# Performance work log

Measured on AMD Instinct MI355X. Metric: run time of the kernel, lower is better.

The kernel has to match this reference:

```python
import jax, jax.numpy as jnp
import numpy as np

B, S, DIN, DIM, H = 2, 2304, 1024, 1024, 16
HEAD_DIM = DIM // H            # 64
ROT_DIM = HEAD_DIM             # partial_rotary_factor = 1
BASE = 10000.0
EPS = 1e-6


def setup_inputs() -> dict:
    key = jax.random.key(0)
    ks = jax.random.split(key, 6)
    return {
        "input": jax.random.normal(ks[0], (B, S, DIN), dtype=jnp.float32),
        "qkv_w": jax.random.normal(ks[1], (3 * DIM, DIN), dtype=jnp.float32) * 0.02,
        "qkv_b": jnp.zeros((3 * DIM,), dtype=jnp.float32),
        "q_scale": jnp.ones((DIM,), dtype=jnp.float32),
        "k_scale": jnp.ones((DIM,), dtype=jnp.float32),
        "proj_w": jax.random.normal(ks[2], (DIN, DIM), dtype=jnp.float32) * 0.02,
        "proj_b": jnp.zeros((DIN,), dtype=jnp.float32),
        "height": 48,
        "width": 48,
    }


def _rms_norm(x, scale):
    # RMSNorm over the full inner dim (QKNorm), learned scale
    var = jnp.mean(x * x, axis=-1, keepdims=True)
    return x * jax.lax.rsqrt(var + EPS) * scale


def _rope_1d(x, pos):
    # x: (b, n, h, d_ax), pos: (n,) float; rotate_half-style RoPE
    d = x.shape[-1]
    inv_freq = 1.0 / (BASE ** (jnp.arange(0, d, 2, dtype=jnp.float32) / d))  # (d/2,)
    ang = pos[:, None] * inv_freq                                            # (n, d/2)
    cos = jnp.concatenate([jnp.cos(ang), jnp.cos(ang)], axis=-1)[None, :, None, :]
    sin = jnp.concatenate([jnp.sin(ang), jnp.sin(ang)], axis=-1)[None, :, None, :]
    x1, x2 = jnp.split(x, 2, axis=-1)
    rot = jnp.concatenate([-x2, x1], axis=-1)
    return x * cos + rot * sin


def _rope_2d(x, height, width):
    # axial 2D RoPE: first half of rotary dims keyed by row, second half by col
    n = height * width
    idx = jnp.arange(n, dtype=jnp.float32)
    rows = jnp.floor(idx / width)
    cols = jnp.mod(idx, width)
    half = ROT_DIM // 2
    x_r = _rope_1d(x[..., :half], rows)
    x_c = _rope_1d(x[..., half:ROT_DIM], cols)
    return jnp.concatenate([x_r, x_c, x[..., ROT_DIM:]], axis=-1)


def reference(input, qkv_w, qkv_b, q_scale, k_scale, proj_w, proj_b, height, width):
    b, n, _ = input.shape
    qkv = input @ qkv_w.T + qkv_b                       # (b, n, 3*dim)
    q, k, v = jnp.split(qkv, 3, axis=-1)
    q = _rms_norm(q, q_scale)
    k = _rms_norm(k, k_scale)
    # (b, n, h, d)
    q = q.reshape(b, n, H, HEAD_DIM)
    k = k.reshape(b, n, H, HEAD_DIM)
    v = v.reshape(b, n, H, HEAD_DIM)
    q = _rope_2d(q, height, width)
    k = _rope_2d(k, height, width)
    scale = HEAD_DIM ** (-0.5)
    # (b, h, q, k)
    scores = jnp.einsum("bqhd,bkhd->bhqk", q, k) * scale
    attn = jax.nn.softmax(scores, axis=-1)
    out = jnp.einsum("bhqk,bkhd->bqhd", attn, v)        # (b, n, h, d)
    out = out.reshape(b, n, DIM)
    return out @ proj_w.T + proj_b
```

## Files before the change

kernel.cpp:

```cpp
#include <hip/hip_runtime.h>
#include <math.h>

#define BB   2
#define SS   2304
#define DINC 1024
#define DIMC 1024
#define HH   16
#define HD   64

typedef _Float16 half_t;
typedef __attribute__((ext_vector_type(4))) _Float16 half4;
typedef __attribute__((ext_vector_type(8))) _Float16 half8;
typedef __attribute__((ext_vector_type(4))) float    f32x4;

#define LOG2E 1.44269504088896340736f
#define EXP2(x) __builtin_amdgcn_exp2f(x)

#define GLOAD_LDS16(gp, lp)                                                     \
    __builtin_amdgcn_global_load_lds(                                           \
        (const __attribute__((address_space(1))) void*)(gp),                    \
        (__attribute__((address_space(3))) void*)(lp), 16, 0, 0)

template<int RB>
__global__ __launch_bounds__(256)
void convert_tile_f16(const float* __restrict__ src, half_t* __restrict__ dst, int K)
{
    constexpr int EPT = RB * 32 / 256;
    const int mb = blockIdx.x;
    const int kb = blockIdx.y;
    const int t  = threadIdx.x;
    const int e0 = t * EPT;
    const int mm = e0 >> 5;
    const int kk = e0 & 31;
    const float* sp = src + (size_t)(mb * RB + mm) * K + kb * 32 + kk;
    half_t*      dp = dst + ((size_t)mb * (K >> 5) + kb) * (RB * 32) + mm * 32 + kk;
    #pragma unroll
    for (int g = 0; g < EPT / 4; ++g) {
        float4 v = *(const float4*)(sp + 4 * g);
        dp[4 * g + 0] = (half_t)v.x; dp[4 * g + 1] = (half_t)v.y;
        dp[4 * g + 2] = (half_t)v.z; dp[4 * g + 3] = (half_t)v.w;
    }
}

template<int BN, bool OUT_HALF>
__global__ __launch_bounds__(256)
void gemm_mfma(const half_t* __restrict__ Ah, const half_t* __restrict__ Bh,
               const float* __restrict__ bias, void* __restrict__ Cout,
               int M, int N, int K)
{
    constexpr int MT = (BN == 128) ? 4 : 2;
    constexpr int NT = 4;
    const int KB = K >> 5;
    __shared__ half_t As[8192];
    __shared__ half_t Bs[2 * BN * 32];

    const int t    = threadIdx.x;
    const int w    = t >> 6;
    const int lane = t & 63;
    const int l15  = lane & 15, quad = lane >> 4;
    const int wr   = (BN == 128) ? (w >> 1) : w;
    const int wc   = (BN == 128) ? (w & 1) : 0;
    const int mb   = blockIdx.y, nb = blockIdx.x;

    f32x4 acc[MT][NT];
    #pragma unroll
    for (int mt = 0; mt < MT; ++mt)
        #pragma unroll
        for (int nt = 0; nt < NT; ++nt) acc[mt][nt] = (f32x4){0.f, 0.f, 0.f, 0.f};

    const half_t* atile = Ah + (size_t)mb * KB * 4096;
    const half_t* btile = Bh + (size_t)nb * KB * (BN * 32);

    for (int kb = 0; kb < KB; kb += 2) {
        #pragma unroll
        for (int u = 0; u < 2; ++u) {
            const half_t* at = atile + (size_t)(kb + u) * 4096;
            const half_t* bt = btile + (size_t)(kb + u) * (BN * 32);
            #pragma unroll
            for (int v = 0; v < 2; ++v) {
                const int ch = w * 2 + v;
                GLOAD_LDS16(at + ch * 512 + lane * 8, As + u * 4096 + ch * 512);
            }
            if (BN == 128) {
                #pragma unroll
                for (int v = 0; v < 2; ++v) {
                    const int ch = w * 2 + v;
                    GLOAD_LDS16(bt + ch * 512 + lane * 8, Bs + u * 4096 + ch * 512);
                }
            } else {
                GLOAD_LDS16(bt + w * 512 + lane * 8, Bs + u * (BN * 32) + w * 512);
            }
        }
        __syncthreads();

        #pragma unroll
        for (int u = 0; u < 2; ++u) {
            half8 af[MT], bf[NT];
            #pragma unroll
            for (int mt = 0; mt < MT; ++mt)
                af[mt] = *(const half8*)(As + u * 4096
                                         + (wr * (MT * 16) + mt * 16 + l15) * 32 + quad * 8);
            #pragma unroll
            for (int nt = 0; nt < NT; ++nt)
                bf[nt] = *(const half8*)(Bs + u * (BN * 32)
                                         + (wc * 64 + nt * 16 + l15) * 32 + quad * 8);
            #pragma unroll
            for (int mt = 0; mt < MT; ++mt)
                #pragma unroll
                for (int nt = 0; nt < NT; ++nt)
                    acc[mt][nt] = __builtin_amdgcn_mfma_f32_16x16x32_f16(
                        af[mt], bf[nt], acc[mt][nt], 0, 0, 0);
        }
        __syncthreads();
    }

    const int bm = mb * 128, bn = nb * BN;
    #pragma unroll
    for (int nt = 0; nt < NT; ++nt) {
        const int n  = bn + wc * 64 + nt * 16 + l15;
        const float bv = bias[n];
        #pragma unroll
        for (int mt = 0; mt < MT; ++mt) {
            const int m0 = bm + wr * (MT * 16) + mt * 16 + quad * 4;
            #pragma unroll
            for (int rg = 0; rg < 4; ++rg) {
                const float v = acc[mt][nt][rg] + bv;
                if (OUT_HALF) ((half_t*)Cout)[(size_t)(m0 + rg) * N + n] = (half_t)v;
                else          ((float*) Cout)[(size_t)(m0 + rg) * N + n] = v;
            }
        }
    }
}

__global__ __launch_bounds__(256)
void normrope_v7(half_t* __restrict__ qkvh, const float* __restrict__ q_scale,
                 const float* __restrict__ k_scale, const int* __restrict__ wptr,
                 half_t* __restrict__ Kf, half_t* __restrict__ Vf)
{
    const int token = blockIdx.x;
    const int s     = token % SS;
    const int b     = token / SS;
    const int w     = *wptr;
    const int t     = threadIdx.x;
    const float rowp = (float)(s / w);
    const float colp = (float)(s % w);

    half_t* base = qkvh + (size_t)token * 3072;

    const int c    = s >> 5;
    const int slot = s & 31;
    const int ktile = (slot >> 2) & 1;
    const int krow  = ((slot >> 3) << 2) + (slot & 3);

    {
        half4 v4 = *(const half4*)(base + 2048 + 4 * t);
        const int dabs0 = 4 * t;
        const int h  = dabs0 >> 6;
        const int sl3 = slot >> 3, sl7 = slot & 7;
        half_t* vdst = Vf + ((size_t)(b * HH + h) * 72 + c) * 2048;
        #pragma unroll
        for (int ii = 0; ii < 4; ++ii) {
            const int d = (dabs0 + ii) & 63;
            vdst[(d >> 4) * 512 + (sl3 * 16 + (d & 15)) * 8 + sl7] = v4[ii];
        }
    }

    __shared__ float buf[DIMC];
    __shared__ float red[4];

    #pragma unroll
    for (int sel = 0; sel < 2; ++sel) {
        half_t* row = base + sel * DIMC;
        const float* scp = sel ? k_scale : q_scale;

        half4 xh = *(const half4*)(row + 4 * t);
        float x0 = (float)xh[0], x1 = (float)xh[1], x2 = (float)xh[2], x3 = (float)xh[3];
        float ss = x0 * x0 + x1 * x1 + x2 * x2 + x3 * x3;
        #pragma unroll
        for (int o = 32; o >= 1; o >>= 1) ss += __shfl_xor(ss, o);
        if ((t & 63) == 0) red[t >> 6] = ss;
        __syncthreads();

        const float rinv = rsqrtf((red[0] + red[1] + red[2] + red[3]) * (1.0f / DIMC) + 1e-6f);
        float4 g = *(const float4*)(scp + 4 * t);
        buf[4 * t + 0] = x0 * rinv * g.x;
        buf[4 * t + 1] = x1 * rinv * g.y;
        buf[4 * t + 2] = x2 * rinv * g.z;
        buf[4 * t + 3] = x3 * rinv * g.w;
        __syncthreads();

        const float qsc = sel ? 1.0f : (0.125f * LOG2E);

        #pragma unroll
        for (int pp = 0; pp < 2; ++pp) {
            const int p = t + pp * 256;
            const int h = p >> 5;
            const int r = p & 31;
            const int j = r & 15;
            const float pos = (r < 16) ? rowp : colp;
            const int d1 = (r < 16) ? j : (32 + j);
            const int d2 = d1 + 16;
            const float freq = exp2f((float)j * -0.83048202372f);
            const float ang  = pos * freq;
            float sn, cs;
            __sincosf(ang, &sn, &cs);
            const float a1 = buf[h * HD + d1], a2 = buf[h * HD + d2];
            const float o1 = (a1 * cs - a2 * sn) * qsc;
            const float o2 = (a2 * cs + a1 * sn) * qsc;
            if (sel == 0) {
                row[h * HD + d1] = (half_t)o1;
                row[h * HD + d2] = (half_t)o2;
            } else {
                half_t* kdst = Kf + ((size_t)(b * HH + h) * 72 + c) * 2048;
                kdst[((ktile << 1) + (d1 >> 5)) * 512
                     + ((((d1 & 31) >> 3) << 4) + krow) * 8 + (d1 & 7)] = (half_t)o1;
                kdst[((ktile << 1) + (d2 >> 5)) * 512
                     + ((((d2 & 31) >> 3) << 4) + krow) * 8 + (d2 & 7)] = (half_t)o2;
            }
        }
        __syncthreads();
    }
}

__global__ __launch_bounds__(256, 4)
void flash_attn_mfma12(const half_t* __restrict__ qkvh, const half_t* __restrict__ Kf,
                       const half_t* __restrict__ Vf, half_t* __restrict__ attn_h)
{
    const int flat = blockIdx.x;
    const int xcd  = flat & 7;
    const int idx  = flat >> 3;
    const int bh   = xcd * 4 + idx / 36;
    const int qtb  = idx % 36;
    const int b    = bh >> 4, h = bh & 15;
    const int t    = threadIdx.x;
    const int w    = t >> 6;
    const int qh   = w >> 1;
    const int jt   = w & 1;
    const int lane = t & 63;
    const int l15  = lane & 15, quad = lane >> 4;

    const size_t tb = (size_t)b * SS;
    const int q0 = qtb * 64;

    __shared__ float mlb[4][32];
    __shared__ float Ob[2][64][33];

    half8 qf[2][2];
    #pragma unroll
    for (int qt = 0; qt < 2; ++qt)
        #pragma unroll
        for (int dg = 0; dg < 2; ++dg)
            qf[qt][dg] = *(const half8*)(qkvh + (tb + q0 + qh * 32 + qt * 16 + l15) * 3072
                                          + h * HD + dg * 32 + quad * 8);

    f32x4 acc[4][2];
    f32x4 lacc[2];
    #pragma unroll
    for (int qt = 0; qt < 2; ++qt) {
        lacc[qt] = (f32x4){0.f, 0.f, 0.f, 0.f};
        #pragma unroll
        for (int dt = 0; dt < 4; ++dt) acc[dt][qt] = (f32x4){0.f, 0.f, 0.f, 0.f};
    }

    const half_t* kpl = Kf + (size_t)bh * 147456 + jt * 2048 + lane * 8;
    const half_t* vpl = Vf + (size_t)bh * 147456 + jt * 2048 + lane * 8;

    half8 k00 = *(const half8*)(kpl);
    half8 k01 = *(const half8*)(kpl + 512);
    half8 k10 = *(const half8*)(kpl + 1024);
    half8 k11 = *(const half8*)(kpl + 1536);
    half8 v0  = *(const half8*)(vpl);
    half8 v1  = *(const half8*)(vpl + 512);
    half8 v2  = *(const half8*)(vpl + 1024);
    half8 v3  = *(const half8*)(vpl + 1536);

    const f32x4 initC = (f32x4){-4.f, -4.f, -4.f, -4.f};

    for (int p = 0; p < 36; ++p) {
        f32x4 scA[2], scB[2];
        __builtin_amdgcn_s_setprio(1);
        #pragma unroll
        for (int qt = 0; qt < 2; ++qt) {
            scA[qt] = initC;
            scA[qt] = __builtin_amdgcn_mfma_f32_16x16x32_f16(k00, qf[qt][0], scA[qt], 0, 0, 0);
            scA[qt] = __builtin_amdgcn_mfma_f32_16x16x32_f16(k01, qf[qt][1], scA[qt], 0, 0, 0);
            scB[qt] = initC;
            scB[qt] = __builtin_amdgcn_mfma_f32_16x16x32_f16(k10, qf[qt][0], scB[qt], 0, 0, 0);
            scB[qt] = __builtin_amdgcn_mfma_f32_16x16x32_f16(k11, qf[qt][1], scB[qt], 0, 0, 0);
        }
        __builtin_amdgcn_s_setprio(0);

        if (p + 1 < 36) {
            const half_t* kN = kpl + (size_t)(p + 1) * 4096;
            k00 = *(const half8*)(kN);
            k01 = *(const half8*)(kN + 512);
            k10 = *(const half8*)(kN + 1024);
            k11 = *(const half8*)(kN + 1536);
        }

        half8 pf[2];
        #pragma unroll
        for (int qt = 0; qt < 2; ++qt) {
            f32x4 eA, eB;
            #pragma unroll
            for (int rg = 0; rg < 4; ++rg) {
                eA[rg] = EXP2(scA[qt][rg]);
                eB[rg] = EXP2(scB[qt][rg]);
            }
            lacc[qt] += eA + eB;
            pf[qt] = (half8){(half_t)eA[0], (half_t)eA[1], (half_t)eA[2], (half_t)eA[3],
                             (half_t)eB[0], (half_t)eB[1], (half_t)eB[2], (half_t)eB[3]};
        }

        __builtin_amdgcn_s_setprio(1);
        #pragma unroll
        for (int dt = 0; dt < 4; ++dt) {
            const half8 vf = (dt == 0) ? v0 : (dt == 1) ? v1 : (dt == 2) ? v2 : v3;
            #pragma unroll
            for (int qt = 0; qt < 2; ++qt)
                acc[dt][qt] = __builtin_amdgcn_mfma_f32_16x16x32_f16(
                    vf, pf[qt], acc[dt][qt], 0, 0, 0);
        }
        __builtin_amdgcn_s_setprio(0);

        if (p + 1 < 36) {
            const half_t* vN = vpl + (size_t)(p + 1) * 4096;
            v0 = *(const half8*)(vN);
            v1 = *(const half8*)(vN + 512);
            v2 = *(const half8*)(vN + 1024);
            v3 = *(const half8*)(vN + 1536);
        }
    }

    #pragma unroll
    for (int qt = 0; qt < 2; ++qt) {
        float lq = (lacc[qt][0] + lacc[qt][1]) + (lacc[qt][2] + lacc[qt][3]);
        lq += __shfl_xor(lq, 16);
        lq += __shfl_xor(lq, 32);
        if (quad == 0) mlb[w][qt * 16 + l15] = lq;
    }
    __syncthreads();

    float fac[2];
    #pragma unroll
    for (int qt = 0; qt < 2; ++qt) {
        const int q = qt * 16 + l15;
        fac[qt] = 1.0f / (mlb[qh * 2 + 0][q] + mlb[qh * 2 + 1][q]);
    }

    #pragma unroll
    for (int ph = 0; ph < 2; ++ph) {
        if (jt == ph) {
            #pragma unroll
            for (int dt = 0; dt < 4; ++dt)
                #pragma unroll
                for (int qt = 0; qt < 2; ++qt)
                    #pragma unroll
                    for (int rg = 0; rg < 4; ++rg) {
                        const int d = dt * 16 + quad * 4 + rg;
                        const int q = qt * 16 + l15;
                        const float v = acc[dt][qt][rg] * fac[qt];
                        if (ph == 0) Ob[qh][d][q] = v;
                        else         Ob[qh][d][q] += v;
                    }
        }
        __syncthreads();
    }

    {
        const int q   = t >> 2;
        const int ds  = (t & 3) * 16;
        const int qh2 = q >> 5, qq = q & 31;
        const size_t mrow = tb + q0 + q;
        const int mb2 = (int)(mrow >> 7);
        const int mm  = (int)(mrow & 127);
        #pragma unroll
        for (int g = 0; g < 4; ++g) {
            const int dd = ds + 4 * g;
            const int kb2 = (h * HD + dd) >> 5;
            const int kk  = dd & 31;
            half4 o;
            o[0] = (half_t)Ob[qh2][dd + 0][qq];
            o[1] = (half_t)Ob[qh2][dd + 1][qq];
            o[2] = (half_t)Ob[qh2][dd + 2][qq];
            o[3] = (half_t)Ob[qh2][dd + 3][qq];
            *(half4*)(attn_h + ((size_t)mb2 * 32 + kb2) * 4096 + mm * 32 + kk) = o;
        }
    }
}

extern "C" void kernel_launch(void* const* d_in, const int* in_sizes, int n_in,
                              void* d_out, int out_size, void* d_ws, size_t ws_size,
                              hipStream_t stream)
{
    const float* input   = (const float*)d_in[0];
    const float* qkv_w   = (const float*)d_in[1];
    const float* qkv_b   = (const float*)d_in[2];
    const float* q_scale = (const float*)d_in[3];
    const float* k_scale = (const float*)d_in[4];
    const float* proj_w  = (const float*)d_in[5];
    const float* proj_b  = (const float*)d_in[6];
    const int*   width   = (const int*)d_in[8];
    float* out = (float*)d_out;

    half_t* qkvh   = (half_t*)d_ws;
    half_t* attn_h = qkvh   + (size_t)4608 * 3072;
    half_t* Vf     = attn_h + (size_t)4608 * 1024;
    half_t* Ah     = Vf     + (size_t)32 * 72 * 2048;
    half_t* Bh1    = Ah     + (size_t)4608 * 1024;
    half_t* Bh2    = Bh1    + (size_t)3072 * 1024;
    half_t* Kf     = Ah;

    const int M = BB * SS;

    convert_tile_f16<128><<<dim3(M / 128, DINC / 32),        256, 0, stream>>>(input,  Ah,  DINC);
    convert_tile_f16<128><<<dim3(3 * DIMC / 128, DINC / 32), 256, 0, stream>>>(qkv_w, Bh1, DINC);
    convert_tile_f16<64><<<dim3(DINC / 64, DIMC / 32),       256, 0, stream>>>(proj_w, Bh2, DIMC);

    gemm_mfma<128, true><<<dim3(3 * DIMC / 128, M / 128), 256, 0, stream>>>(
        Ah, Bh1, qkv_b, qkvh, M, 3 * DIMC, DINC);

    normrope_v7<<<M, 256, 0, stream>>>(qkvh, q_scale, k_scale, width, Kf, Vf);

    flash_attn_mfma12<<<dim3(1152), 256, 0, stream>>>(qkvh, Kf, Vf, attn_h);

    gemm_mfma<64, false><<<dim3(DINC / 64, M / 128), 256, 0, stream>>>(
        attn_h, Bh2, proj_b, out, M, DINC, DIMC);
}
```

Measured before the change: 245.3 us.

## Software-pipeline QK MFMAs ahead of PV and compute row sums via MFMA

Restructures the attention loop so that the next tile's score MFMAs are issued while the current tile's exponentials are consumed, with K fragments prefetched two iterations ahead. The softmax denominator is now accumulated with an extra MFMA against a ones-row operand instead of VALU adds and cross-lane shuffles. This aims to overlap the exp/VALU work with matrix-core work and reduce VALU load, at the cost of more live registers and two extra MFMAs per iteration.

```diff
diff --git a/kernel.cpp b/kernel.cpp
--- a/kernel.cpp
+++ b/kernel.cpp
@@ -223,7 +223,7 @@
 }
 
 __global__ __launch_bounds__(256, 4)
-void flash_attn_mfma12(const half_t* __restrict__ qkvh, const half_t* __restrict__ Kf,
+void flash_attn_mfma13(const half_t* __restrict__ qkvh, const half_t* __restrict__ Kf,
                        const half_t* __restrict__ Vf, half_t* __restrict__ attn_h)
 {
     const int flat = blockIdx.x;
@@ -253,11 +253,17 @@
             qf[qt][dg] = *(const half8*)(qkvh + (tb + q0 + qh * 32 + qt * 16 + l15) * 3072
                                           + h * HD + dg * 32 + quad * 8);
 
+    const half8 onesA = (l15 == 0)
+        ? (half8){(half_t)1, (half_t)1, (half_t)1, (half_t)1,
+                  (half_t)1, (half_t)1, (half_t)1, (half_t)1}
+        : (half8){(half_t)0, (half_t)0, (half_t)0, (half_t)0,
+                  (half_t)0, (half_t)0, (half_t)0, (half_t)0};
+
     f32x4 acc[4][2];
-    f32x4 lacc[2];
+    f32x4 acc5[2];
     #pragma unroll
     for (int qt = 0; qt < 2; ++qt) {
-        lacc[qt] = (f32x4){0.f, 0.f, 0.f, 0.f};
+        acc5[qt] = (f32x4){0.f, 0.f, 0.f, 0.f};
         #pragma unroll
         for (int dt = 0; dt < 4; ++dt) acc[dt][qt] = (f32x4){0.f, 0.f, 0.f, 0.f};
     }
@@ -276,42 +282,62 @@
 
     const f32x4 initC = (f32x4){-4.f, -4.f, -4.f, -4.f};
 
+    f32x4 scA[2], scB[2];
+    __builtin_amdgcn_s_setprio(1);
+    #pragma unroll
+    for (int qt = 0; qt < 2; ++qt) {
+        scA[qt] = initC;
+        scA[qt] = __builtin_amdgcn_mfma_f32_16x16x32_f16(k00, qf[qt][0], scA[qt], 0, 0, 0);
+        scA[qt] = __builtin_amdgcn_mfma_f32_16x16x32_f16(k01, qf[qt][1], scA[qt], 0, 0, 0);
+        scB[qt] = initC;
+        scB[qt] = __builtin_amdgcn_mfma_f32_16x16x32_f16(k10, qf[qt][0], scB[qt], 0, 0, 0);
+        scB[qt] = __builtin_amdgcn_mfma_f32_16x16x32_f16(k11, qf[qt][1], scB[qt], 0, 0, 0);
+    }
+    __builtin_amdgcn_s_setprio(0);
+    {
+        const half_t* kN = kpl + 4096;
+        k00 = *(const half8*)(kN);
+        k01 = *(const half8*)(kN + 512);
+        k10 = *(const half8*)(kN + 1024);
+        k11 = *(const half8*)(kN + 1536);
+    }
+
     for (int p = 0; p < 36; ++p) {
-        f32x4 scA[2], scB[2];
-        __builtin_amdgcn_s_setprio(1);
+        half8 pf[2];
         #pragma unroll
         for (int qt = 0; qt < 2; ++qt) {
-            scA[qt] = initC;
-            scA[qt] = __builtin_amdgcn_mfma_f32_16x16x32_f16(k00, qf[qt][0], scA[qt], 0, 0, 0);
-            scA[qt] = __builtin_amdgcn_mfma_f32_16x16x32_f16(k01, qf[qt][1], scA[qt], 0, 0, 0);
-            scB[qt] = initC;
-            scB[qt] = __builtin_amdgcn_mfma_f32_16x16x32_f16(k10, qf[qt][0], scB[qt], 0, 0, 0);
-            scB[qt] = __builtin_amdgcn_mfma_f32_16x16x32_f16(k11, qf[qt][1], scB[qt], 0, 0, 0);
-        }
-        __builtin_amdgcn_s_setprio(0);
+            f32x4 eA, eB;
+            #pragma unroll
+            for (int rg = 0; rg < 4; ++rg) {
+                eA[rg] = EXP2(scA[qt][rg]);
+                eB[rg] = EXP2(scB[qt][rg]);
+            }
+            pf[qt] = (half8){(half_t)eA[0], (half_t)eA[1], (half_t)eA[2], (half_t)eA[3],
+                             (half_t)eB[0], (half_t)eB[1], (half_t)eB[2], (half_t)eB[3]};
+        }
 
         if (p + 1 < 36) {
-            const half_t* kN = kpl + (size_t)(p + 1) * 4096;
+            __builtin_amdgcn_s_setprio(1);
+            #pragma unroll
+            for (int qt = 0; qt < 2; ++qt) {
+                scA[qt] = initC;
+                scA[qt] = __builtin_amdgcn_mfma_f32_16x16x32_f16(k00, qf[qt][0], scA[qt], 0, 0, 0);
+                scA[qt] = __builtin_amdgcn_mfma_f32_16x16x32_f16(k01, qf[qt][1], scA[qt], 0, 0, 0);
+                scB[qt] = initC;
+                scB[qt] = __builtin_amdgcn_mfma_f32_16x16x32_f16(k10, qf[qt][0], scB[qt], 0, 0, 0);
+                scB[qt] = __builtin_amdgcn_mfma_f32_16x16x32_f16(k11, qf[qt][1], scB[qt], 0, 0, 0);
+            }
+            __builtin_amdgcn_s_setprio(0);
+        }
+
+        if (p + 2 < 36) {
+            const half_t* kN = kpl + (size_t)(p + 2) * 4096;
             k00 = *(const half8*)(kN);
             k01 = *(const half8*)(kN + 512);
             k10 = *(const half8*)(kN + 1024);
             k11 = *(const half8*)(kN + 1536);
         }
 
-        half8 pf[2];
-        #pragma unroll
-        for (int qt = 0; qt < 2; ++qt) {
-            f32x4 eA, eB;
-            #pragma unroll
-            for (int rg = 0; rg < 4; ++rg) {
-                eA[rg] = EXP2(scA[qt][rg]);
-                eB[rg] = EXP2(scB[qt][rg]);
-            }
-            lacc[qt] += eA + eB;
-            pf[qt] = (half8){(half_t)eA[0], (half_t)eA[1], (half_t)eA[2], (half_t)eA[3],
-                             (half_t)eB[0], (half_t)eB[1], (half_t)eB[2], (half_t)eB[3]};
-        }
-
         __builtin_amdgcn_s_setprio(1);
         #pragma unroll
         for (int dt = 0; dt < 4; ++dt) {
@@ -321,6 +347,10 @@
                 acc[dt][qt] = __builtin_amdgcn_mfma_f32_16x16x32_f16(
                     vf, pf[qt], acc[dt][qt], 0, 0, 0);
         }
+        #pragma unroll
+        for (int qt = 0; qt < 2; ++qt)
+            acc5[qt] = __builtin_amdgcn_mfma_f32_16x16x32_f16(
+                onesA, pf[qt], acc5[qt], 0, 0, 0);
         __builtin_amdgcn_s_setprio(0);
 
         if (p + 1 < 36) {
@@ -333,12 +363,8 @@
     }
 
     #pragma unroll
-    for (int qt = 0; qt < 2; ++qt) {
-        float lq = (lacc[qt][0] + lacc[qt][1]) + (lacc[qt][2] + lacc[qt][3]);
-        lq += __shfl_xor(lq, 16);
-        lq += __shfl_xor(lq, 32);
-        if (quad == 0) mlb[w][qt * 16 + l15] = lq;
-    }
+    for (int qt = 0; qt < 2; ++qt)
+        if (quad == 0) mlb[w][qt * 16 + l15] = acc5[qt][0];
     __syncthreads();
 
     float fac[2];
@@ -422,7 +448,7 @@
 
     normrope_v7<<<M, 256, 0, stream>>>(qkvh, q_scale, k_scale, width, Kf, Vf);
 
-    flash_attn_mfma12<<<dim3(1152), 256, 0, stream>>>(qkvh, Kf, Vf, attn_h);
+    flash_attn_mfma13<<<dim3(1152), 256, 0, stream>>>(qkvh, Kf, Vf, attn_h);
 
     gemm_mfma<64, false><<<dim3(DINC / 64, M / 128), 256, 0, stream>>>(
         attn_h, Bh2, proj_b, out, M, DINC, DIMC);
```

After: 257.4 us. 1.05x slower.

## Stage K/V tiles through double-buffered LDS with direct global-to-LDS loads

Applied to the files above, without the earlier changes.

Replaces per-wave direct global register loads of K and V with a cooperative scheme where each wave copies one quarter of the K/V tile into a double-buffered LDS stage via global_load_lds, then all waves read their fragments from LDS. This removes the duplicated global fetches between waves sharing the same key tile and lets the next tile's load overlap the current compute. It adds a block-wide barrier per iteration and LDS reads, and reuses the stage buffer for the output reduction scratch.

```diff
diff --git a/kernel.cpp b/kernel.cpp
--- a/kernel.cpp
+++ b/kernel.cpp
@@ -223,7 +223,7 @@
 }
 
 __global__ __launch_bounds__(256, 4)
-void flash_attn_mfma12(const half_t* __restrict__ qkvh, const half_t* __restrict__ Kf,
+void flash_attn_mfma14(const half_t* __restrict__ qkvh, const half_t* __restrict__ Kf,
                        const half_t* __restrict__ Vf, half_t* __restrict__ attn_h)
 {
     const int flat = blockIdx.x;
@@ -242,8 +242,9 @@
     const size_t tb = (size_t)b * SS;
     const int q0 = qtb * 64;
 
+    __shared__ __align__(16) half_t stage[2][4][2048];
     __shared__ float mlb[4][32];
-    __shared__ float Ob[2][64][33];
+    float (*Ob)[64][33] = reinterpret_cast<float (*)[64][33]>(&stage[0][0][0]);
 
     half8 qf[2][2];
     #pragma unroll
@@ -262,21 +263,41 @@
         for (int dt = 0; dt < 4; ++dt) acc[dt][qt] = (f32x4){0.f, 0.f, 0.f, 0.f};
     }
 
-    const half_t* kpl = Kf + (size_t)bh * 147456 + jt * 2048 + lane * 8;
-    const half_t* vpl = Vf + (size_t)bh * 147456 + jt * 2048 + lane * 8;
-
-    half8 k00 = *(const half8*)(kpl);
-    half8 k01 = *(const half8*)(kpl + 512);
-    half8 k10 = *(const half8*)(kpl + 1024);
-    half8 k11 = *(const half8*)(kpl + 1536);
-    half8 v0  = *(const half8*)(vpl);
-    half8 v1  = *(const half8*)(vpl + 512);
-    half8 v2  = *(const half8*)(vpl + 1024);
-    half8 v3  = *(const half8*)(vpl + 1536);
+    const half_t* srcb = ((w & 2) ? Vf : Kf) + (size_t)bh * 147456;
+    const int spar = w & 1;
+
+    {
+        const half_t* sp = srcb + spar * 2048 + lane * 8;
+        half_t* dp = &stage[0][w][0];
+        #pragma unroll
+        for (int g = 0; g < 4; ++g)
+            GLOAD_LDS16(sp + g * 512, dp + g * 512);
+    }
+    __syncthreads();
 
     const f32x4 initC = (f32x4){-4.f, -4.f, -4.f, -4.f};
+    int u = 0;
 
     for (int p = 0; p < 36; ++p) {
+        if (p + 1 < 36) {
+            const half_t* sp = srcb + (size_t)(p + 1) * 4096 + spar * 2048 + lane * 8;
+            half_t* dp = &stage[u ^ 1][w][0];
+            #pragma unroll
+            for (int g = 0; g < 4; ++g)
+                GLOAD_LDS16(sp + g * 512, dp + g * 512);
+        }
+
+        const half_t* kl = &stage[u][jt][0] + lane * 8;
+        const half_t* vl = &stage[u][2 + jt][0] + lane * 8;
+        half8 k00 = *(const half8*)(kl);
+        half8 k01 = *(const half8*)(kl + 512);
+        half8 k10 = *(const half8*)(kl + 1024);
+        half8 k11 = *(const half8*)(kl + 1536);
+        half8 v0  = *(const half8*)(vl);
+        half8 v1  = *(const half8*)(vl + 512);
+        half8 v2  = *(const half8*)(vl + 1024);
+        half8 v3  = *(const half8*)(vl + 1536);
+
         f32x4 scA[2], scB[2];
         __builtin_amdgcn_s_setprio(1);
         #pragma unroll
@@ -290,14 +311,6 @@
         }
         __builtin_amdgcn_s_setprio(0);
 
-        if (p + 1 < 36) {
-            const half_t* kN = kpl + (size_t)(p + 1) * 4096;
-            k00 = *(const half8*)(kN);
-            k01 = *(const half8*)(kN + 512);
-            k10 = *(const half8*)(kN + 1024);
-            k11 = *(const half8*)(kN + 1536);
-        }
-
         half8 pf[2];
         #pragma unroll
         for (int qt = 0; qt < 2; ++qt) {
@@ -323,13 +336,8 @@
         }
         __builtin_amdgcn_s_setprio(0);
 
-        if (p + 1 < 36) {
-            const half_t* vN = vpl + (size_t)(p + 1) * 4096;
-            v0 = *(const half8*)(vN);
-            v1 = *(const half8*)(vN + 512);
-            v2 = *(const half8*)(vN + 1024);
-            v3 = *(const half8*)(vN + 1536);
-        }
+        __syncthreads();
+        u ^= 1;
     }
 
     #pragma unroll
@@ -422,7 +430,7 @@
 
     normrope_v7<<<M, 256, 0, stream>>>(qkvh, q_scale, k_scale, width, Kf, Vf);
 
-    flash_attn_mfma12<<<dim3(1152), 256, 0, stream>>>(qkvh, Kf, Vf, attn_h);
+    flash_attn_mfma14<<<dim3(1152), 256, 0, stream>>>(qkvh, Kf, Vf, attn_h);
 
     gemm_mfma<64, false><<<dim3(DINC / 64, M / 128), 256, 0, stream>>>(
         attn_h, Bh2, proj_b, out, M, DINC, DIMC);
```

After: 258.0 us. 5.2% more time.
